# Performance work log

Hardware: AMD Instinct MI355X
Metric: run time of the kernel (lower is better)

Reference implementation:

```python
import jax, jax.numpy as jnp
import numpy as np

B = 256
D, H, W = 15, 64, 128    # depth, latitude, longitude of input grid
d, h, w = 5, 16, 32      # grid after AveragePooling3D(3,4,4)
L_DEPTH = (d + 2) * h * w      # 3584
L_LON   = d * h * (w + 2)      # 2720
L_LAT   = d * (h + 2) * w      # 2880


def _local1d(xp, wt, bias):
    # Unshared-weight LocallyConnected1D(filters=1, kernel=3) + relu.
    # xp: (B, L+2) padded sequence; wt: (L, 3); bias: (L,)
    L = wt.shape[0]
    y = (wt[:, 0] * xp[:, 0:L]
         + wt[:, 1] * xp[:, 1:L + 1]
         + wt[:, 2] * xp[:, 2:L + 2]
         + bias)
    return jax.nn.relu(y)


def setup_inputs() -> dict:
    key = jax.random.key(0)
    ks = jax.random.split(key, 7)
    s = 0.1
    return {
        "x": jax.random.normal(ks[0], (B, D, H, W, 1), jnp.float32),
        "w_depth": jax.random.normal(ks[1], (L_DEPTH, 3), jnp.float32) * s,
        "b_depth": jax.random.normal(ks[2], (L_DEPTH,), jnp.float32) * s,
        "w_lon": jax.random.normal(ks[3], (L_LON, 3), jnp.float32) * s,
        "b_lon": jax.random.normal(ks[4], (L_LON,), jnp.float32) * s,
        "w_lat": jax.random.normal(ks[5], (L_LAT, 3), jnp.float32) * s,
        "b_lat": jax.random.normal(ks[6], (L_LAT,), jnp.float32) * s,
    }


def reference(x, w_depth, b_depth, w_lon, b_lon, w_lat, b_lat):
    Bn = x.shape[0]
    # AveragePooling3D(3,4,4): dims divide evenly -> reshape + mean
    xs = x.reshape(Bn, d, 3, h, 4, w, 4, 1).mean(axis=(2, 4, 6))  # (B,d,h,w,1)

    # ---- depth axis: pad depth, permute (3,2,1,4), flatten, local conv ----
    t = jnp.pad(xs, ((0, 0), (1, 1), (0, 0), (0, 0), (0, 0)))     # (B,d+2,h,w,1)
    t = jnp.transpose(t, (0, 3, 2, 1, 4))                         # (B,w,h,d+2,1)
    t = t.reshape(Bn, L_DEPTH)
    t = jnp.pad(t, ((0, 0), (1, 1)))                              # ZeroPadding1D(1)
    t = _local1d(t, w_depth, b_depth)
    t = t.reshape(Bn, w, h, d + 2, 1)
    t = jnp.transpose(t, (0, 3, 2, 1, 4))                         # (B,d+2,h,w,1)
    t = t[:, 1:-1]                                                # crop depth -> (B,d,h,w,1)

    # ---- longitude axis: pad last spatial dim, identity permute ----
    u = jnp.pad(t, ((0, 0), (0, 0), (0, 0), (1, 1), (0, 0)))      # (B,d,h,w+2,1)
    u = u.reshape(Bn, L_LON)
    u = jnp.pad(u, ((0, 0), (1, 1)))
    u = _local1d(u, w_lon, b_lon)
    u = u.reshape(Bn, d, h, w + 2, 1)
    u = u[:, :, :, 1:-1]                                          # (B,d,h,w,1)

    # ---- latitude axis: pad lat, permute (1,3,2,4) ----
    v = jnp.pad(u, ((0, 0), (0, 0), (1, 1), (0, 0), (0, 0)))      # (B,d,h+2,w,1)
    v = jnp.transpose(v, (0, 1, 3, 2, 4))                         # (B,d,w,h+2,1)
    v = v.reshape(Bn, L_LAT)
    v = jnp.pad(v, ((0, 0), (1, 1)))
    v = _local1d(v, w_lat, b_lat)
    v = v.reshape(Bn, d, w, h + 2, 1)
    v = jnp.transpose(v, (0, 1, 3, 2, 4))                         # (B,d,h+2,w,1)
    v = v[:, :, 1:-1]                                             # (B,d,h,w,1)

    # UpSampling3D(3,4,4): nearest-neighbor repeat
    out = jnp.broadcast_to(
        v[:, :, None, :, None, :, None, :],
        (Bn, d, 3, h, 4, w, 4, 1)
    ).reshape(Bn, D, H, W, 1)
    return out
```

## Files before the change

kernel.cpp:

```cpp
#include <hip/hip_runtime.h>


#define THREADS 1024
#define NELEM   (15 * 64 * 128)

__global__ __launch_bounds__(THREADS) void localnet_kernel(
    const float* __restrict__ x,
    const float* __restrict__ w_depth, const float* __restrict__ b_depth,
    const float* __restrict__ w_lon,   const float* __restrict__ b_lon,
    const float* __restrict__ w_lat,   const float* __restrict__ b_lat,
    float* __restrict__ out)
{
    const int b   = blockIdx.x;
    const int tid = threadIdx.x;

    __shared__ float bufA[3586];
    __shared__ float bufB[3584];

    const float* xb = x   + (size_t)b * NELEM;
    float*       ob = out + (size_t)b * NELEM;

    for (int i = tid; i < 3586; i += THREADS) bufA[i] = 0.f;
    __syncthreads();

    for (int c = tid; c < 2560; c += THREADS) {
        const int iw = c & 31;
        const int ih = (c >> 5) & 15;
        const int id = c >> 9;
        const float* p = xb + ((id * 3) * 64 + ih * 4) * 128 + iw * 4;
        float s = 0.f;
        #pragma unroll
        for (int dd = 0; dd < 3; ++dd) {
            #pragma unroll
            for (int hh = 0; hh < 4; ++hh) {
                const float4 v = *reinterpret_cast<const float4*>(p + (dd * 64 + hh) * 128);
                s += (v.x + v.y) + (v.z + v.w);
            }
        }
        bufA[1 + ((iw * 16 + ih) * 7 + (id + 1))] = s * (1.f / 48.f);
    }
    __syncthreads();

    for (int l = tid; l < 3584; l += THREADS) {
        float y = w_depth[l * 3 + 0] * bufA[l]
                + w_depth[l * 3 + 1] * bufA[l + 1]
                + w_depth[l * 3 + 2] * bufA[l + 2]
                + b_depth[l];
        bufB[l] = fmaxf(y, 0.f);
    }
    __syncthreads();

    for (int i = tid; i < 2722; i += THREADS) {
        float v = 0.f;
        if (i >= 1 && i <= 2720) {
            const int l   = i - 1;
            const int k   = l % 34;
            const int ih  = (l / 34) & 15;
            const int dep = l / (34 * 16);
            if (k >= 1 && k <= 32)
                v = bufB[((k - 1) * 16 + ih) * 7 + dep + 1];
        }
        bufA[i] = v;
    }
    __syncthreads();

    for (int l = tid; l < 2720; l += THREADS) {
        float y = w_lon[l * 3 + 0] * bufA[l]
                + w_lon[l * 3 + 1] * bufA[l + 1]
                + w_lon[l * 3 + 2] * bufA[l + 2]
                + b_lon[l];
        bufB[l] = fmaxf(y, 0.f);
    }
    __syncthreads();

    for (int i = tid; i < 2882; i += THREADS) {
        float v = 0.f;
        if (i >= 1 && i <= 2880) {
            const int l   = i - 1;
            const int k   = l % 18;
            const int iw  = (l / 18) & 31;
            const int dep = l / (18 * 32);
            if (k >= 1 && k <= 16)
                v = bufB[(dep * 16 + (k - 1)) * 34 + iw + 1];
        }
        bufA[i] = v;
    }
    __syncthreads();

    for (int l = tid; l < 2880; l += THREADS) {
        float y = w_lat[l * 3 + 0] * bufA[l]
                + w_lat[l * 3 + 1] * bufA[l + 1]
                + w_lat[l * 3 + 2] * bufA[l + 2]
                + b_lat[l];
        bufB[l] = fmaxf(y, 0.f);
    }
    __syncthreads();

    for (int o = tid; o < 30720; o += THREADS) {
        const int iw4 = o & 31;
        const int Hin = (o >> 5) & 63;
        const int Din = o >> 11;
        const float v = bufB[((Din / 3) * 32 + iw4) * 18 + (Hin >> 2) + 1];
        *reinterpret_cast<float4*>(ob + (size_t)o * 4) = make_float4(v, v, v, v);
    }
}

extern "C" void kernel_launch(void* const* d_in, const int* in_sizes, int n_in,
                              void* d_out, int out_size, void* d_ws, size_t ws_size,
                              hipStream_t stream) {
    const float* x       = (const float*)d_in[0];
    const float* w_depth = (const float*)d_in[1];
    const float* b_depth = (const float*)d_in[2];
    const float* w_lon   = (const float*)d_in[3];
    const float* b_lon   = (const float*)d_in[4];
    const float* w_lat   = (const float*)d_in[5];
    const float* b_lat   = (const float*)d_in[6];
    float* out = (float*)d_out;

    const int Bn = in_sizes[0] / NELEM;
    localnet_kernel<<<dim3(Bn), dim3(THREADS), 0, stream>>>(
        x, w_depth, b_depth, w_lon, b_lon, w_lat, b_lat, out);
}
```

Baseline: 251.4 us.

## Split fused kernel into downsample, conv and upsample kernels for parallelism

Splits the single per-batch kernel into three launches: a grid-wide average-pooling kernel, a per-batch shared-memory conv chain, and a grid-wide nearest-neighbour upsampling kernel. The previous design ran only 256 blocks, which limited memory-level parallelism for the large input read and output write. The new design adds two extra launches and a round trip through workspace memory for the small intermediate tensors.

```diff
diff --git a/kernel.cpp b/kernel.cpp
--- a/kernel.cpp
+++ b/kernel.cpp
@@ -1,47 +1,59 @@
 #include <hip/hip_runtime.h>
 
 
-#define THREADS 1024
 #define NELEM   (15 * 64 * 128)
+#define NCELL   2560
+#define NQ      30720
 
-__global__ __launch_bounds__(THREADS) void localnet_kernel(
-    const float* __restrict__ x,
+__global__ __launch_bounds__(256) void k_down(const float* __restrict__ x,
+                                              float* __restrict__ ds)
+{
+    const int idx = blockIdx.x * 256 + threadIdx.x;
+    const int b   = idx >> 11 >> 0;
+    const int bb  = idx / NCELL;
+    const int c   = idx - bb * NCELL;
+    const int iw  = c & 31;
+    const int ih  = (c >> 5) & 15;
+    const int id  = c >> 9;
+
+    const float* p = x + (size_t)bb * NELEM + ((id * 3) * 64 + ih * 4) * 128 + iw * 4;
+    float s = 0.f;
+    #pragma unroll
+    for (int dd = 0; dd < 3; ++dd) {
+        #pragma unroll
+        for (int hh = 0; hh < 4; ++hh) {
+            const float4 v = *reinterpret_cast<const float4*>(p + (dd * 64 + hh) * 128);
+            s += (v.x + v.y) + (v.z + v.w);
+        }
+    }
+    ds[idx] = s * (1.f / 48.f);
+    (void)b;
+}
+
+__global__ __launch_bounds__(256) void k_conv(
+    const float* __restrict__ ds,
     const float* __restrict__ w_depth, const float* __restrict__ b_depth,
     const float* __restrict__ w_lon,   const float* __restrict__ b_lon,
     const float* __restrict__ w_lat,   const float* __restrict__ b_lat,
-    float* __restrict__ out)
+    float* __restrict__ v2)
 {
     const int b   = blockIdx.x;
     const int tid = threadIdx.x;
-
     __shared__ float bufA[3586];
     __shared__ float bufB[3584];
 
-    const float* xb = x   + (size_t)b * NELEM;
-    float*       ob = out + (size_t)b * NELEM;
-
-    for (int i = tid; i < 3586; i += THREADS) bufA[i] = 0.f;
+    for (int i = tid; i < 3586; i += 256) bufA[i] = 0.f;
     __syncthreads();
 
-    for (int c = tid; c < 2560; c += THREADS) {
+    for (int c = tid; c < NCELL; c += 256) {
         const int iw = c & 31;
         const int ih = (c >> 5) & 15;
         const int id = c >> 9;
-        const float* p = xb + ((id * 3) * 64 + ih * 4) * 128 + iw * 4;
-        float s = 0.f;
-        #pragma unroll
-        for (int dd = 0; dd < 3; ++dd) {
-            #pragma unroll
-            for (int hh = 0; hh < 4; ++hh) {
-                const float4 v = *reinterpret_cast<const float4*>(p + (dd * 64 + hh) * 128);
-                s += (v.x + v.y) + (v.z + v.w);
-            }
-        }
-        bufA[1 + ((iw * 16 + ih) * 7 + (id + 1))] = s * (1.f / 48.f);
+        bufA[1 + ((iw * 16 + ih) * 7 + id + 1)] = ds[(size_t)b * NCELL + c];
     }
     __syncthreads();
 
-    for (int l = tid; l < 3584; l += THREADS) {
+    for (int l = tid; l < 3584; l += 256) {
         float y = w_depth[l * 3 + 0] * bufA[l]
                 + w_depth[l * 3 + 1] * bufA[l + 1]
                 + w_depth[l * 3 + 2] * bufA[l + 2]
@@ -50,7 +62,7 @@
     }
     __syncthreads();
 
-    for (int i = tid; i < 2722; i += THREADS) {
+    for (int i = tid; i < 2722; i += 256) {
         float v = 0.f;
         if (i >= 1 && i <= 2720) {
             const int l   = i - 1;
@@ -64,7 +76,7 @@
     }
     __syncthreads();
 
-    for (int l = tid; l < 2720; l += THREADS) {
+    for (int l = tid; l < 2720; l += 256) {
         float y = w_lon[l * 3 + 0] * bufA[l]
                 + w_lon[l * 3 + 1] * bufA[l + 1]
                 + w_lon[l * 3 + 2] * bufA[l + 2]
@@ -73,7 +85,7 @@
     }
     __syncthreads();
 
-    for (int i = tid; i < 2882; i += THREADS) {
+    for (int i = tid; i < 2882; i += 256) {
         float v = 0.f;
         if (i >= 1 && i <= 2880) {
             const int l   = i - 1;
@@ -87,7 +99,7 @@
     }
     __syncthreads();
 
-    for (int l = tid; l < 2880; l += THREADS) {
+    for (int l = tid; l < 2880; l += 256) {
         float y = w_lat[l * 3 + 0] * bufA[l]
                 + w_lat[l * 3 + 1] * bufA[l + 1]
                 + w_lat[l * 3 + 2] * bufA[l + 2]
@@ -96,13 +108,27 @@
     }
     __syncthreads();
 
-    for (int o = tid; o < 30720; o += THREADS) {
-        const int iw4 = o & 31;
-        const int Hin = (o >> 5) & 63;
-        const int Din = o >> 11;
-        const float v = bufB[((Din / 3) * 32 + iw4) * 18 + (Hin >> 2) + 1];
-        *reinterpret_cast<float4*>(ob + (size_t)o * 4) = make_float4(v, v, v, v);
+    for (int c = tid; c < NCELL; c += 256) {
+        const int iww = c & 31;
+        const int ihh = (c >> 5) & 15;
+        const int dep = c >> 9;
+        v2[(size_t)b * NCELL + c] = bufB[(dep * 32 + iww) * 18 + ihh + 1];
     }
+}
+
+__global__ __launch_bounds__(256) void k_up(const float* __restrict__ v2,
+                                            float* __restrict__ out)
+{
+    const int idx = blockIdx.x * 256 + threadIdx.x;
+    const int b   = idx / NQ;
+    const int o   = idx - b * NQ;
+    const int iw4 = o & 31;
+    const int Hin = (o >> 5) & 63;
+    const int Din = o >> 11;
+
+    const float v = v2[(size_t)b * NCELL + ((Din / 3) * 16 + (Hin >> 2)) * 32 + iw4];
+    *reinterpret_cast<float4*>(out + (size_t)b * NELEM + (size_t)o * 4) =
+        make_float4(v, v, v, v);
 }
 
 extern "C" void kernel_launch(void* const* d_in, const int* in_sizes, int n_in,
@@ -118,6 +144,12 @@
     float* out = (float*)d_out;
 
     const int Bn = in_sizes[0] / NELEM;
-    localnet_kernel<<<dim3(Bn), dim3(THREADS), 0, stream>>>(
-        x, w_depth, b_depth, w_lon, b_lon, w_lat, b_lat, out);
+
+    float* ds = (float*)d_ws;
+    float* v2 = ds + (size_t)Bn * NCELL;
+
+    k_down<<<dim3(Bn * NCELL / 256), dim3(256), 0, stream>>>(x, ds);
+    k_conv<<<dim3(Bn), dim3(256), 0, stream>>>(ds, w_depth, b_depth,
+                                               w_lon, b_lon, w_lat, b_lat, v2);
+    k_up<<<dim3(Bn * NQ / 256), dim3(256), 0, stream>>>(v2, out);
 }
```

Result: no change. 250.1 us (-0.5%).

## Split fused per-batch kernel into four grid-parallel kernels via workspace

Applied to the files above, without the earlier changes.

Replaces the single kernel, which ran one 1024-thread block per batch item with shared-memory staging, with four kernels: downsample, depth conv, longitude conv, and latitude conv fused with upsampling. Intermediates go through global workspace, and each kernel uses a 2D grid over batch and positions so there are many more blocks to spread across the GPU. The intent is to remove the low parallelism of only 256 blocks and the many block-wide barriers. The cost is three extra launches, global-memory round trips for intermediates, and recomputing the latitude conv for every output float4.

```diff
diff --git a/kernel.cpp b/kernel.cpp
--- a/kernel.cpp
+++ b/kernel.cpp
@@ -1,108 +1,116 @@
 #include <hip/hip_runtime.h>
 
 
-#define THREADS 1024
-#define NELEM   (15 * 64 * 128)
+#define NELEM (15 * 64 * 128)
+#define NCELL 2560
+#define LD    3584
+#define LLON  2720
+#define LLAT  2880
 
-__global__ __launch_bounds__(THREADS) void localnet_kernel(
-    const float* __restrict__ x,
-    const float* __restrict__ w_depth, const float* __restrict__ b_depth,
-    const float* __restrict__ w_lon,   const float* __restrict__ b_lon,
-    const float* __restrict__ w_lat,   const float* __restrict__ b_lat,
-    float* __restrict__ out)
+__global__ __launch_bounds__(256) void k_down(const float* __restrict__ x,
+                                              float* __restrict__ ds)
 {
-    const int b   = blockIdx.x;
-    const int tid = threadIdx.x;
+    const int b  = blockIdx.y;
+    const int c  = blockIdx.x * 256 + threadIdx.x;
+    const int iw = c & 31;
+    const int ih = (c >> 5) & 15;
+    const int id = c >> 9;
 
-    __shared__ float bufA[3586];
-    __shared__ float bufB[3584];
+    const float* p = x + (size_t)b * NELEM + ((id * 3) * 64 + ih * 4) * 128 + iw * 4;
+    float s = 0.f;
+    #pragma unroll
+    for (int dd = 0; dd < 3; ++dd) {
+        #pragma unroll
+        for (int hh = 0; hh < 4; ++hh) {
+            const float4 v = *reinterpret_cast<const float4*>(p + (dd * 64 + hh) * 128);
+            s += (v.x + v.y) + (v.z + v.w);
+        }
+    }
+    ds[(size_t)b * NCELL + c] = s * (1.f / 48.f);
+}
 
-    const float* xb = x   + (size_t)b * NELEM;
-    float*       ob = out + (size_t)b * NELEM;
+__device__ __forceinline__ float tf_depth(const float* __restrict__ dsb, int f)
+{
+    const int k  = f % 7;
+    const int q  = f / 7;
+    const int ih = q & 15;
+    const int iw = q >> 4;
+    return (k >= 1 && k <= 5) ? dsb[((k - 1) * 16 + ih) * 32 + iw] : 0.f;
+}
 
-    for (int i = tid; i < 3586; i += THREADS) bufA[i] = 0.f;
-    __syncthreads();
+__global__ __launch_bounds__(256) void k_depth(const float* __restrict__ ds,
+                                               const float* __restrict__ w,
+                                               const float* __restrict__ bias,
+                                               float* __restrict__ t1)
+{
+    const int b = blockIdx.y;
+    const int l = blockIdx.x * 256 + threadIdx.x;
+    const float* dsb = ds + (size_t)b * NCELL;
 
-    for (int c = tid; c < 2560; c += THREADS) {
-        const int iw = c & 31;
-        const int ih = (c >> 5) & 15;
-        const int id = c >> 9;
-        const float* p = xb + ((id * 3) * 64 + ih * 4) * 128 + iw * 4;
-        float s = 0.f;
-        #pragma unroll
-        for (int dd = 0; dd < 3; ++dd) {
-            #pragma unroll
-            for (int hh = 0; hh < 4; ++hh) {
-                const float4 v = *reinterpret_cast<const float4*>(p + (dd * 64 + hh) * 128);
-                s += (v.x + v.y) + (v.z + v.w);
-            }
-        }
-        bufA[1 + ((iw * 16 + ih) * 7 + (id + 1))] = s * (1.f / 48.f);
-    }
-    __syncthreads();
+    const float x0 = (l > 0)      ? tf_depth(dsb, l - 1) : 0.f;
+    const float x1 =                tf_depth(dsb, l);
+    const float x2 = (l < LD - 1) ? tf_depth(dsb, l + 1) : 0.f;
+    const float y  = w[l * 3] * x0 + w[l * 3 + 1] * x1 + w[l * 3 + 2] * x2 + bias[l];
+    t1[(size_t)b * LD + l] = fmaxf(y, 0.f);
+}
 
-    for (int l = tid; l < 3584; l += THREADS) {
-        float y = w_depth[l * 3 + 0] * bufA[l]
-                + w_depth[l * 3 + 1] * bufA[l + 1]
-                + w_depth[l * 3 + 2] * bufA[l + 2]
-                + b_depth[l];
-        bufB[l] = fmaxf(y, 0.f);
-    }
-    __syncthreads();
+__device__ __forceinline__ float uf_lon(const float* __restrict__ t1b, int f)
+{
+    const int kw  = f % 34;
+    const int q   = f / 34;
+    const int ih  = q & 15;
+    const int dep = q >> 4;
+    return (kw >= 1 && kw <= 32) ? t1b[((kw - 1) * 16 + ih) * 7 + dep + 1] : 0.f;
+}
 
-    for (int i = tid; i < 2722; i += THREADS) {
-        float v = 0.f;
-        if (i >= 1 && i <= 2720) {
-            const int l   = i - 1;
-            const int k   = l % 34;
-            const int ih  = (l / 34) & 15;
-            const int dep = l / (34 * 16);
-            if (k >= 1 && k <= 32)
-                v = bufB[((k - 1) * 16 + ih) * 7 + dep + 1];
-        }
-        bufA[i] = v;
-    }
-    __syncthreads();
+__global__ __launch_bounds__(256) void k_lon(const float* __restrict__ t1,
+                                             const float* __restrict__ w,
+                                             const float* __restrict__ bias,
+                                             float* __restrict__ u1)
+{
+    const int b = blockIdx.y;
+    const int m = blockIdx.x * 256 + threadIdx.x;
+    if (m >= LLON) return;
+    const float* t1b = t1 + (size_t)b * LD;
 
-    for (int l = tid; l < 2720; l += THREADS) {
-        float y = w_lon[l * 3 + 0] * bufA[l]
-                + w_lon[l * 3 + 1] * bufA[l + 1]
-                + w_lon[l * 3 + 2] * bufA[l + 2]
-                + b_lon[l];
-        bufB[l] = fmaxf(y, 0.f);
-    }
-    __syncthreads();
+    const float x0 = (m > 0)        ? uf_lon(t1b, m - 1) : 0.f;
+    const float x1 =                  uf_lon(t1b, m);
+    const float x2 = (m < LLON - 1) ? uf_lon(t1b, m + 1) : 0.f;
+    const float y  = w[m * 3] * x0 + w[m * 3 + 1] * x1 + w[m * 3 + 2] * x2 + bias[m];
+    u1[(size_t)b * LLON + m] = fmaxf(y, 0.f);
+}
 
-    for (int i = tid; i < 2882; i += THREADS) {
-        float v = 0.f;
-        if (i >= 1 && i <= 2880) {
-            const int l   = i - 1;
-            const int k   = l % 18;
-            const int iw  = (l / 18) & 31;
-            const int dep = l / (18 * 32);
-            if (k >= 1 && k <= 16)
-                v = bufB[(dep * 16 + (k - 1)) * 34 + iw + 1];
-        }
-        bufA[i] = v;
-    }
-    __syncthreads();
+__device__ __forceinline__ float vf_lat(const float* __restrict__ u1b, int f)
+{
+    const int kh  = f % 18;
+    const int q   = f / 18;
+    const int iw  = q & 31;
+    const int dep = q >> 5;
+    return (kh >= 1 && kh <= 16) ? u1b[(dep * 16 + kh - 1) * 34 + iw + 1] : 0.f;
+}
 
-    for (int l = tid; l < 2880; l += THREADS) {
-        float y = w_lat[l * 3 + 0] * bufA[l]
-                + w_lat[l * 3 + 1] * bufA[l + 1]
-                + w_lat[l * 3 + 2] * bufA[l + 2]
-                + b_lat[l];
-        bufB[l] = fmaxf(y, 0.f);
-    }
-    __syncthreads();
+__global__ __launch_bounds__(256) void k_lat_up(const float* __restrict__ u1,
+                                                const float* __restrict__ w,
+                                                const float* __restrict__ bias,
+                                                float* __restrict__ out)
+{
+    const int b   = blockIdx.y;
+    const int o   = blockIdx.x * 256 + threadIdx.x;
+    const int iww = o & 31;
+    const int Hin = (o >> 5) & 63;
+    const int Din = o >> 11;
+    const int dep = Din / 3;
+    const int ihh = Hin >> 2;
+    const int n   = (dep * 32 + iww) * 18 + ihh + 1;
 
-    for (int o = tid; o < 30720; o += THREADS) {
-        const int iw4 = o & 31;
-        const int Hin = (o >> 5) & 63;
-        const int Din = o >> 11;
-        const float v = bufB[((Din / 3) * 32 + iw4) * 18 + (Hin >> 2) + 1];
-        *reinterpret_cast<float4*>(ob + (size_t)o * 4) = make_float4(v, v, v, v);
-    }
+    const float* u1b = u1 + (size_t)b * LLON;
+    const float x0 = vf_lat(u1b, n - 1);
+    const float x1 = vf_lat(u1b, n);
+    const float x2 = vf_lat(u1b, n + 1);
+    const float y  = fmaxf(w[n * 3] * x0 + w[n * 3 + 1] * x1 + w[n * 3 + 2] * x2 + bias[n], 0.f);
+
+    *reinterpret_cast<float4*>(out + (size_t)b * NELEM + (size_t)o * 4) =
+        make_float4(y, y, y, y);
 }
 
 extern "C" void kernel_launch(void* const* d_in, const int* in_sizes, int n_in,
@@ -118,6 +126,13 @@
     float* out = (float*)d_out;
 
     const int Bn = in_sizes[0] / NELEM;
-    localnet_kernel<<<dim3(Bn), dim3(THREADS), 0, stream>>>(
-        x, w_depth, b_depth, w_lon, b_lon, w_lat, b_lat, out);
+
+    float* ds = (float*)d_ws;
+    float* t1 = ds + (size_t)Bn * NCELL;
+    float* u1 = t1 + (size_t)Bn * LD;
+
+    k_down  <<<dim3(NCELL / 256, Bn), dim3(256), 0, stream>>>(x, ds);
+    k_depth <<<dim3(LD / 256, Bn),    dim3(256), 0, stream>>>(ds, w_depth, b_depth, t1);
+    k_lon   <<<dim3((LLON + 255) / 256, Bn), dim3(256), 0, stream>>>(t1, w_lon, b_lon, u1);
+    k_lat_up<<<dim3(NELEM / 4 / 256, Bn), dim3(256), 0, stream>>>(u1, w_lat, b_lat, out);
 }
```

Measured after the change: 247.1 us. About the same (-1.7%).
